# Kernel tuning notes

Hardware: AMD Instinct MI355X
Metric: run time of the kernel (lower is better)

## Reference

```python
import jax, jax.numpy as jnp
import numpy as np

N, D, L, H = 4, 512, 2048, 8  # batch, feat_dim, seq_len, num_heads


def setup_inputs() -> dict:
    key = jax.random.key(0)
    k1, k2, k3, k4 = jax.random.split(key, 4)
    x = jax.random.normal(k1, (N, D, L), dtype=jnp.float32)
    w_qkv = jax.random.normal(k2, (3 * D, D, 1), dtype=jnp.float32) * 0.02   # 1x1 conv
    w_dw = jax.random.normal(k3, (3 * D, 1, 3), dtype=jnp.float32) * 0.02    # depthwise k=3
    w_proj = jax.random.normal(k4, (D, D, 1), dtype=jnp.float32) * 0.02      # 1x1 conv
    temperature = jnp.ones((1, H, 1, 1), dtype=jnp.float32)
    return {"x": x, "w_qkv": w_qkv, "w_dw": w_dw, "w_proj": w_proj, "temperature": temperature}


def _conv1x1(x, w):
    # x: (n, c_in, l), w: (c_out, c_in, 1)
    return jnp.einsum('oc,ncl->nol', w[:, :, 0], x)


def _l2norm(t, eps=1e-12):
    # matches F.normalize: t / max(||t||_2, eps) along last dim
    n = jnp.sqrt(jnp.sum(t * t, axis=-1, keepdims=True))
    return t / jnp.maximum(n, eps)


def reference(x, w_qkv, w_dw, w_proj, temperature):
    n, d, l = x.shape
    h = temperature.shape[1]
    dh = d // h

    qkv = _conv1x1(x, w_qkv)                               # (n, 3d, l)
    qkv = jax.lax.conv_general_dilated(
        qkv, w_dw, window_strides=(1,), padding=[(1, 1)],
        dimension_numbers=('NCH', 'OIH', 'NCH'),
        feature_group_count=3 * d)                          # depthwise conv, (n, 3d, l)

    q, k, v = jnp.split(qkv, 3, axis=1)                     # each (n, d, l)
    # (n, d, l) -> (n, h, dh, l) -> (n, h, l, dh)
    q = q.reshape(n, h, dh, l).transpose(0, 1, 3, 2)
    k = k.reshape(n, h, dh, l).transpose(0, 1, 3, 2)
    v = v.reshape(n, h, dh, l).transpose(0, 1, 3, 2)

    q = _l2norm(q)
    k = _l2norm(k)

    scores = jnp.einsum('nhqd,nhkd->nhqk', q, k) * temperature  # (n, h, l, l)
    attn = jax.nn.softmax(scores, axis=-1)
    out = jnp.einsum('nhqk,nhkd->nhqd', attn, v)                # (n, h, l, dh)
    out = out.transpose(0, 1, 3, 2).reshape(n, d, l)            # (n, d, l)
    return _conv1x1(out, w_proj)
```

## Files before the change

kernel.cpp:

```cpp
#include <hip/hip_runtime.h>
#include <hip/hip_bf16.h>
#include <cstdint>
#include <cstddef>

#define N_B 4
#define D_F 512
#define L_S 2048
#define H_N 8
#define DH  64
#define C3  (3*D_F)

typedef __attribute__((ext_vector_type(8)))  short short8;
typedef __attribute__((ext_vector_type(4)))  float f32x4;
typedef __attribute__((ext_vector_type(16))) float f32x16;

__device__ __forceinline__ unsigned int pk_bf16(float a, float b) {
    __hip_bfloat162 h = __float22bfloat162_rn(float2{a, b});
    union { __hip_bfloat162 h; unsigned int u; } cv;
    cv.h = h;
    return cv.u;
}
__device__ __forceinline__ unsigned short bf16_rn(float f) {
    union { float f; unsigned int u; } c; c.f = f;
    unsigned int r = c.u + 0x7FFF + ((c.u >> 16) & 1);
    return (unsigned short)(r >> 16);
}
__device__ __forceinline__ float bf16_f(unsigned short h) {
    union { unsigned int u; float f; } c; c.u = ((unsigned int)h) << 16;
    return c.f;
}

__device__ __forceinline__ void gll16(const unsigned short* g, unsigned short* l) {
    __builtin_amdgcn_global_load_lds(
        (const __attribute__((address_space(1))) unsigned int*)g,
        (__attribute__((address_space(3))) unsigned int*)l,
        16, 0, 0);
}

__global__ __launch_bounds__(256) void cvt_split(const float* __restrict__ src,
                                                 unsigned short* __restrict__ hi,
                                                 unsigned short* __restrict__ lo,
                                                 int n4) {
    int i = blockIdx.x * 256 + threadIdx.x;
    if (i >= n4) return;
    float4 v = ((const float4*)src)[i];
    ushort4 h, l;
    h.x = bf16_rn(v.x); l.x = bf16_rn(v.x - bf16_f(h.x));
    h.y = bf16_rn(v.y); l.y = bf16_rn(v.y - bf16_f(h.y));
    h.z = bf16_rn(v.z); l.z = bf16_rn(v.z - bf16_f(h.z));
    h.w = bf16_rn(v.w); l.w = bf16_rn(v.w - bf16_f(h.w));
    ((ushort4*)hi)[i] = h;
    ((ushort4*)lo)[i] = l;
}

__global__ __launch_bounds__(256) void cvt_xT(const float* __restrict__ x,
                                              unsigned short* __restrict__ xT,
                                              int C) {
    __shared__ float tile[64][65];
    const int tid = threadIdx.x;
    const int l0  = blockIdx.x * 64;
    const int c0  = blockIdx.y * 64;
    const int n   = blockIdx.z;

    const float* xn = x + (size_t)n * C * L_S;
#pragma unroll
    for (int r = 0; r < 16; ++r) {
        int c = r * 4 + (tid >> 6);
        int l = tid & 63;
        tile[c][l] = xn[(size_t)(c0 + c) * L_S + l0 + l];
    }
    __syncthreads();

    unsigned short* xn_t = xT + (size_t)n * L_S * C;
#pragma unroll
    for (int r = 0; r < 8; ++r) {
        int l  = r * 8 + (tid >> 5);
        int cp = tid & 31;
        unsigned int pk = pk_bf16(tile[cp * 2][l], tile[cp * 2 + 1][l]);
        *(unsigned int*)&xn_t[(size_t)(l0 + l) * C + c0 + cp * 2] = pk;
    }
}

template<int SPLIT, int OUT_BF16>
__global__ __launch_bounds__(256) void gemm_mfma2(const unsigned short* __restrict__ Whi,
                                                  const unsigned short* __restrict__ Wlo,
                                                  const unsigned short* __restrict__ XThi,
                                                  const unsigned short* __restrict__ XTlo,
                                                  void* __restrict__ Y,
                                                  int O, int C) {
    __shared__ unsigned short Wt[SPLIT ? 2 : 1][4][128 * 8];
    __shared__ unsigned short Xt[SPLIT ? 2 : 1][4][128 * 8];

    const int tid  = threadIdx.x;
    const int lane = tid & 63;
    const int w    = tid >> 6;
    const int g    = lane >> 4;
    const int c    = lane & 15;
    const int wr   = (w >> 1) * 64;
    const int wc   = (w & 1) * 64;
    const int l0   = blockIdx.x * 128;
    const int o0   = blockIdx.y * 128;
    const int n    = blockIdx.z;

    const unsigned short* XTn_hi = XThi + (size_t)n * L_S * C;
    const unsigned short* XTn_lo = SPLIT ? (XTlo + (size_t)n * L_S * C) : nullptr;

    const int rhalf = (w & 1) * 64;
    const int cpA   = w >> 1;
    const int cpB   = 2 + (w >> 1);
    const size_t wrowA = (size_t)(o0 + rhalf + lane) * C;
    const size_t xrowA = (size_t)(l0 + rhalf + lane) * C;

    f32x4 acc[4][4];
#pragma unroll
    for (int mt = 0; mt < 4; ++mt)
#pragma unroll
        for (int nt = 0; nt < 4; ++nt) acc[mt][nt] = (f32x4){0.f, 0.f, 0.f, 0.f};

    for (int c0 = 0; c0 < C; c0 += 32) {
        __syncthreads();
        gll16(Whi + wrowA + c0 + cpA * 8, &Wt[0][cpA][rhalf * 8]);
        gll16(Whi + wrowA + c0 + cpB * 8, &Wt[0][cpB][rhalf * 8]);
        gll16(XTn_hi + xrowA + c0 + cpA * 8, &Xt[0][cpA][rhalf * 8]);
        gll16(XTn_hi + xrowA + c0 + cpB * 8, &Xt[0][cpB][rhalf * 8]);
        if (SPLIT) {
            gll16(Wlo + wrowA + c0 + cpA * 8, &Wt[1][cpA][rhalf * 8]);
            gll16(Wlo + wrowA + c0 + cpB * 8, &Wt[1][cpB][rhalf * 8]);
            gll16(XTn_lo + xrowA + c0 + cpA * 8, &Xt[1][cpA][rhalf * 8]);
            gll16(XTn_lo + xrowA + c0 + cpB * 8, &Xt[1][cpB][rhalf * 8]);
        }
        __syncthreads();

        short8 a0[4], b0[4];
#pragma unroll
        for (int mt = 0; mt < 4; ++mt) a0[mt] = *(short8*)&Wt[0][g][(wr + mt * 16 + c) * 8];
#pragma unroll
        for (int nt = 0; nt < 4; ++nt) b0[nt] = *(short8*)&Xt[0][g][(wc + nt * 16 + c) * 8];

        if (SPLIT) {
            short8 a1[4], b1[4];
#pragma unroll
            for (int mt = 0; mt < 4; ++mt) a1[mt] = *(short8*)&Wt[1][g][(wr + mt * 16 + c) * 8];
#pragma unroll
            for (int nt = 0; nt < 4; ++nt) b1[nt] = *(short8*)&Xt[1][g][(wc + nt * 16 + c) * 8];
#pragma unroll
            for (int mt = 0; mt < 4; ++mt)
#pragma unroll
                for (int nt = 0; nt < 4; ++nt) {
                    acc[mt][nt] = __builtin_amdgcn_mfma_f32_16x16x32_bf16(a0[mt], b0[nt], acc[mt][nt], 0, 0, 0);
                    acc[mt][nt] = __builtin_amdgcn_mfma_f32_16x16x32_bf16(a0[mt], b1[nt], acc[mt][nt], 0, 0, 0);
                    acc[mt][nt] = __builtin_amdgcn_mfma_f32_16x16x32_bf16(a1[mt], b0[nt], acc[mt][nt], 0, 0, 0);
                }
        } else {
#pragma unroll
            for (int mt = 0; mt < 4; ++mt)
#pragma unroll
                for (int nt = 0; nt < 4; ++nt)
                    acc[mt][nt] = __builtin_amdgcn_mfma_f32_16x16x32_bf16(a0[mt], b0[nt], acc[mt][nt], 0, 0, 0);
        }
    }

#pragma unroll
    for (int mt = 0; mt < 4; ++mt) {
#pragma unroll
        for (int r = 0; r < 4; ++r) {
            int oo = o0 + wr + mt * 16 + g * 4 + r;
            size_t rowbase = ((size_t)n * O + oo) * L_S;
#pragma unroll
            for (int nt = 0; nt < 4; ++nt) {
                int ll = l0 + wc + nt * 16 + c;
                if (OUT_BF16)
                    ((unsigned short*)Y)[rowbase + ll] = bf16_rn(acc[mt][nt][r]);
                else
                    ((float*)Y)[rowbase + ll] = acc[mt][nt][r];
            }
        }
    }
}

__global__ __launch_bounds__(256) void fused_qk2(const unsigned short* __restrict__ qkv_bf,
                                                 const float* __restrict__ w_dw,
                                                 unsigned short* __restrict__ Qb,
                                                 unsigned short* __restrict__ Kb) {
    __shared__ unsigned short rows[64 * 264];
    __shared__ float wsm[192];
    const int tid = threadIdx.x;
    const int l0  = blockIdx.x * 256;
    const int gg  = blockIdx.y;
    const int n   = blockIdx.z;
    const int head = gg & 7;
    const int ch0  = (gg < 8) ? head * 64 : 512 + head * 64;

    if (tid < 192) wsm[tid] = w_dw[ch0 * 3 + tid];

    const unsigned short* base = qkv_bf + ((size_t)n * C3 + ch0) * L_S;
    for (int f = tid; f < 2048; f += 256) {
        int e = f >> 5, s = f & 31;
        *(uint4*)&rows[e * 264 + s * 8] = *(const uint4*)&base[(size_t)e * L_S + l0 + s * 8];
    }
    if (tid < 64) {
        rows[tid * 264 + 256] = (l0 > 0) ? base[(size_t)tid * L_S + l0 - 1] : (unsigned short)0;
    } else if (tid < 128) {
        int e = tid - 64;
        rows[e * 264 + 257] = (l0 + 256 < L_S) ? base[(size_t)e * L_S + l0 + 256] : (unsigned short)0;
    }
    __syncthreads();

    const int lL = tid;
    const int iL = (lL == 0)   ? 256 : lL - 1;
    const int iR = (lL == 255) ? 257 : lL + 1;
    float y[64];
    float s = 0.f;
#pragma unroll
    for (int e = 0; e < 64; ++e) {
        float a = bf16_f(rows[e * 264 + iL]);
        float b = bf16_f(rows[e * 264 + lL]);
        float d = bf16_f(rows[e * 264 + iR]);
        float v = wsm[e * 3 + 0] * a + wsm[e * 3 + 1] * b + wsm[e * 3 + 2] * d;
        y[e] = v;
        s += v * v;
    }
    float sc = 1.0f / fmaxf(sqrtf(s), 1e-12f);

    const int l = l0 + tid;
    unsigned short* dst = ((gg < 8) ? Qb : Kb) + (size_t)(n * H_N + head) * 8 * L_S * 8;
#pragma unroll
    for (int p = 0; p < 8; ++p) {
        uint4 pk = make_uint4(pk_bf16(y[8 * p + 0] * sc, y[8 * p + 1] * sc),
                              pk_bf16(y[8 * p + 2] * sc, y[8 * p + 3] * sc),
                              pk_bf16(y[8 * p + 4] * sc, y[8 * p + 5] * sc),
                              pk_bf16(y[8 * p + 6] * sc, y[8 * p + 7] * sc));
        *(uint4*)&dst[((size_t)p * L_S + l) * 8] = pk;
    }
}

__global__ __launch_bounds__(256) void fused_v2(const unsigned short* __restrict__ qkv_bf,
                                                const float* __restrict__ w_dw,
                                                unsigned short* __restrict__ Vb) {
    const int tid = threadIdx.x;
    const int e   = tid & 63;
    const int jp  = blockIdx.x * 4 + (tid >> 6);
    const int h   = blockIdx.y;
    const int n   = blockIdx.z;
    const int ch  = 1024 + h * 64 + e;
    const unsigned short* row = qkv_bf + ((size_t)n * C3 + ch) * L_S;
    const int k0 = jp * 8;

    uint4 mv = *(const uint4*)&row[k0];
    unsigned int lw = (jp > 0)   ? *(const unsigned int*)&row[k0 - 2] : 0u;
    unsigned int rw = (jp < 255) ? *(const unsigned int*)&row[k0 + 8] : 0u;

    float v[10];
    v[0] = bf16_f((unsigned short)(lw >> 16));
    v[1] = bf16_f((unsigned short)(mv.x & 0xFFFF));
    v[2] = bf16_f((unsigned short)(mv.x >> 16));
    v[3] = bf16_f((unsigned short)(mv.y & 0xFFFF));
    v[4] = bf16_f((unsigned short)(mv.y >> 16));
    v[5] = bf16_f((unsigned short)(mv.z & 0xFFFF));
    v[6] = bf16_f((unsigned short)(mv.z >> 16));
    v[7] = bf16_f((unsigned short)(mv.w & 0xFFFF));
    v[8] = bf16_f((unsigned short)(mv.w >> 16));
    v[9] = bf16_f((unsigned short)(rw & 0xFFFF));

    float w0 = w_dw[ch * 3 + 0], w1 = w_dw[ch * 3 + 1], w2 = w_dw[ch * 3 + 2];
    unsigned int o[4];
#pragma unroll
    for (int i = 0; i < 4; ++i) {
        float y0 = w0 * v[2 * i + 0] + w1 * v[2 * i + 1] + w2 * v[2 * i + 2];
        float y1 = w0 * v[2 * i + 1] + w1 * v[2 * i + 2] + w2 * v[2 * i + 3];
        o[i] = pk_bf16(y0, y1);
    }
    uint4 ov = make_uint4(o[0], o[1], o[2], o[3]);
    *(uint4*)&Vb[(((size_t)(n * H_N + h) * 256 + jp) * 512) + e * 8] = ov;
}

__global__ __launch_bounds__(512, 2) void attn9(const unsigned short* __restrict__ Qb,
                                                const unsigned short* __restrict__ Kb,
                                                const unsigned short* __restrict__ Vb,
                                                const float* __restrict__ temp,
                                                unsigned short* __restrict__ aoT_hi,
                                                unsigned short* __restrict__ aoT_lo) {
    __shared__ float Ot[128 * 64];
    __shared__ float smB[128];
    __shared__ float smA[128];

    const int tid  = threadIdx.x;
    const int lane = tid & 63;
    const int w    = tid >> 6;
    const int g2   = w >> 2;
    const int wv   = w & 3;
    const int c32  = lane & 31;
    const int h    = lane >> 5;
    const int q0   = blockIdx.x * 128;
    const int hd   = blockIdx.y;
    const int n    = blockIdx.z;

    const size_t hb = (size_t)(n * H_N + hd);
    const unsigned short* Qh = Qb + hb * 8 * L_S * 8;
    const unsigned short* Kh = Kb + hb * 8 * L_S * 8;
    const unsigned short* Vh = Vb + hb * 256 * 512;
    const float t    = temp[hd];
    const float negm = -fabsf(t);

    short8 qa[4];
#pragma unroll
    for (int es = 0; es < 4; ++es)
        qa[es] = *(const short8*)&Qh[((size_t)(es * 2 + h) * L_S + q0 + wv * 32 + c32) * 8];

    f32x16 acc0, acc1;
#pragma unroll
    for (int i = 0; i < 16; ++i) { acc0[i] = 0.f; acc1[i] = 0.f; }
    float sumP = 0.f;

    for (int it = 0; it < 16; ++it) {
        const int k0 = (it * 2 + g2) * 64;

        short8 vb0[4], vb1[4];
#pragma unroll
        for (int ks = 0; ks < 4; ++ks) {
            const unsigned short* vrow = Vh + (size_t)((k0 >> 3) + ks * 2 + h) * 512;
            vb0[ks] = *(const short8*)&vrow[c32 * 8];
            vb1[ks] = *(const short8*)&vrow[(32 + c32) * 8];
        }

        f32x16 sf0, sf1;
#pragma unroll
        for (int i = 0; i < 16; ++i) { sf0[i] = 0.f; sf1[i] = 0.f; }
        short8 ka0[4], ka1[4];
#pragma unroll
        for (int es = 0; es < 4; ++es) {
            const unsigned short* krow = Kh + (size_t)(es * 2 + h) * L_S * 8;
            ka0[es] = *(const short8*)&krow[(k0 + c32) * 8];
            ka1[es] = *(const short8*)&krow[(k0 + 32 + c32) * 8];
        }
        __builtin_amdgcn_s_setprio(1);
#pragma unroll
        for (int es = 0; es < 4; ++es) {
            sf0 = __builtin_amdgcn_mfma_f32_32x32x16_bf16(ka0[es], qa[es], sf0, 0, 0, 0);
            sf1 = __builtin_amdgcn_mfma_f32_32x32x16_bf16(ka1[es], qa[es], sf1, 0, 0, 0);
        }
        __builtin_amdgcn_s_setprio(0);

        short8 pa[4];
        {
            unsigned int W_[16], R_[16];
#pragma unroll
            for (int G = 0; G < 4; ++G) {
                float p0 = __expf(fmaf(sf0[4*G+0], t, negm));
                float p1 = __expf(fmaf(sf0[4*G+1], t, negm));
                float p2 = __expf(fmaf(sf0[4*G+2], t, negm));
                float p3 = __expf(fmaf(sf0[4*G+3], t, negm));
                sumP += (p0 + p1) + (p2 + p3);
                W_[2*G]   = pk_bf16(p0, p1);
                W_[2*G+1] = pk_bf16(p2, p3);
                float u0 = __expf(fmaf(sf1[4*G+0], t, negm));
                float u1 = __expf(fmaf(sf1[4*G+1], t, negm));
                float u2 = __expf(fmaf(sf1[4*G+2], t, negm));
                float u3 = __expf(fmaf(sf1[4*G+3], t, negm));
                sumP += (u0 + u1) + (u2 + u3);
                W_[8+2*G]   = pk_bf16(u0, u1);
                W_[8+2*G+1] = pk_bf16(u2, u3);
            }
#pragma unroll
            for (int j = 0; j < 16; ++j) R_[j] = __shfl_xor(W_[j], 32);
#pragma unroll
            for (int ks = 0; ks < 4; ++ks) {
                const int bb = (ks >> 1) * 8;
                const int m4 = (ks & 1) * 4;
                unsigned int a0 = h ? R_[bb+m4+2] : W_[bb+m4+0];
                unsigned int a1 = h ? R_[bb+m4+3] : W_[bb+m4+1];
                unsigned int a2 = h ? W_[bb+m4+2] : R_[bb+m4+0];
                unsigned int a3 = h ? W_[bb+m4+3] : R_[bb+m4+1];
                uint4 pu = make_uint4(a0, a1, a2, a3);
                pa[ks] = *(short8*)&pu;
            }
        }

        __builtin_amdgcn_s_setprio(1);
#pragma unroll
        for (int ks = 0; ks < 4; ++ks) {
            acc0 = __builtin_amdgcn_mfma_f32_32x32x16_bf16(pa[ks], vb0[ks], acc0, 0, 0, 0);
            acc1 = __builtin_amdgcn_mfma_f32_32x32x16_bf16(pa[ks], vb1[ks], acc1, 0, 0, 0);
        }
        __builtin_amdgcn_s_setprio(0);
    }

    sumP += __shfl_xor(sumP, 32);

    if (g2 == 1) {
        smB[wv * 32 + c32] = sumP;
#pragma unroll
        for (int r = 0; r < 16; ++r) {
            int ql = (r & 3) + 8 * (r >> 2) + 4 * h;
            int qg = wv * 32 + ql;
            Ot[qg * 64 + c32]      = acc0[r];
            Ot[qg * 64 + 32 + c32] = acc1[r];
        }
    } else {
        smA[wv * 32 + c32] = sumP;
    }
    __syncthreads();

    if (g2 == 0) {
        float b0[16], b1[16], inv[16];
#pragma unroll
        for (int r = 0; r < 16; ++r) {
            int ql = (r & 3) + 8 * (r >> 2) + 4 * h;
            int qg = wv * 32 + ql;
            b0[r] = Ot[qg * 64 + c32];
            b1[r] = Ot[qg * 64 + 32 + c32];
            inv[r] = 1.0f / (smA[qg] + smB[qg]);
        }
#pragma unroll
        for (int r = 0; r < 16; ++r) {
            int ql = (r & 3) + 8 * (r >> 2) + 4 * h;
            int qg = wv * 32 + ql;
            Ot[qg * 64 + (c32 ^ (qg & 31))]        = (acc0[r] + b0[r]) * inv[r];
            Ot[qg * 64 + ((32 + c32) ^ (qg & 31))] = (acc1[r] + b1[r]) * inv[r];
        }
    }
    __syncthreads();

    for (int tt = tid; tt < 8192; tt += 512) {
        int qq = tt >> 6, e = tt & 63;
        float v = Ot[qq * 64 + (e ^ (qq & 31))];
        unsigned short hi_ = bf16_rn(v);
        unsigned short lo_ = bf16_rn(v - bf16_f(hi_));
        size_t off = ((size_t)n * L_S + q0 + qq) * D_F + hd * 64 + e;
        aoT_hi[off] = hi_;
        aoT_lo[off] = lo_;
    }
}

extern "C" void kernel_launch(void* const* d_in, const int* in_sizes, int n_in,
                              void* d_out, int out_size, void* d_ws, size_t ws_size,
                              hipStream_t stream) {
    const float* x      = (const float*)d_in[0];
    const float* w_qkv  = (const float*)d_in[1];
    const float* w_dw   = (const float*)d_in[2];
    const float* w_proj = (const float*)d_in[3];
    const float* temp   = (const float*)d_in[4];
    float* out = (float*)d_out;

    const size_t WQE = (size_t)C3 * D_F;
    const size_t WPE = (size_t)D_F * D_F;

    char* ws = (char*)d_ws;
    unsigned short* qkv_bf = (unsigned short*)ws;
    unsigned short* Qb     = (unsigned short*)(ws + 25165824);
    unsigned short* Kb     = (unsigned short*)(ws + 33554432);
    unsigned short* Vb     = (unsigned short*)(ws + 41943040);
    unsigned short* xT     = (unsigned short*)(ws + 50331648);
    unsigned short* aoT_lo = (unsigned short*)(ws + 58720256);
    unsigned short* wq_hi  = (unsigned short*)(ws + 67108864);
    unsigned short* wq_lo  = wq_hi + WQE;
    unsigned short* wp_hi  = (unsigned short*)(ws + 70254592);
    unsigned short* wp_lo  = wp_hi + WPE;
    unsigned short* aoT_hi = xT;

    cvt_xT<<<dim3(L_S / 64, D_F / 64, N_B), 256, 0, stream>>>(x, xT, D_F);
    cvt_split<<<dim3((WQE / 4 + 255) / 256), 256, 0, stream>>>(w_qkv, wq_hi, wq_lo, WQE / 4);
    cvt_split<<<dim3((WPE / 4 + 255) / 256), 256, 0, stream>>>(w_proj, wp_hi, wp_lo, WPE / 4);

    gemm_mfma2<0, 1><<<dim3(L_S / 128, C3 / 128, N_B), 256, 0, stream>>>(
        wq_hi, nullptr, xT, nullptr, qkv_bf, C3, D_F);

    fused_qk2<<<dim3(L_S / 256, 16, N_B), 256, 0, stream>>>(qkv_bf, w_dw, Qb, Kb);
    fused_v2<<<dim3(64, H_N, N_B), 256, 0, stream>>>(qkv_bf, w_dw, Vb);

    attn9<<<dim3(L_S / 128, H_N, N_B), 512, 0, stream>>>(Qb, Kb, Vb, temp, aoT_hi, aoT_lo);

    gemm_mfma2<1, 0><<<dim3(L_S / 128, D_F / 128, N_B), 256, 0, stream>>>(
        wp_hi, wp_lo, aoT_hi, aoT_lo, out, D_F, D_F);
}
```

Baseline: 157.4 us.

## Use permlane32_swap for P relayout, raise attention occupancy, merge weight conversions

The attention kernel replaces the 16 cross-half __shfl_xor exchanges used to rearrange softmax probabilities into MFMA A-operand layout with permlane32_swap instructions. A runtime probe determines the swap direction semantics, so the R_ register array is no longer needed. Launch bounds are raised from 2 to 4 blocks per CU, which forces a tighter register budget and risks spills. The two weight-conversion kernels are also merged into one launch to cut launch overhead.

```diff
diff --git a/kernel.cpp b/kernel.cpp
--- a/kernel.cpp
+++ b/kernel.cpp
@@ -37,20 +37,29 @@
         16, 0, 0);
 }
 
-__global__ __launch_bounds__(256) void cvt_split(const float* __restrict__ src,
-                                                 unsigned short* __restrict__ hi,
-                                                 unsigned short* __restrict__ lo,
-                                                 int n4) {
+__global__ __launch_bounds__(256) void cvt_split_w(const float* __restrict__ wq,
+                                                   unsigned short* __restrict__ wq_hi,
+                                                   unsigned short* __restrict__ wq_lo,
+                                                   int n4q,
+                                                   const float* __restrict__ wp,
+                                                   unsigned short* __restrict__ wp_hi,
+                                                   unsigned short* __restrict__ wp_lo,
+                                                   int n4p) {
     int i = blockIdx.x * 256 + threadIdx.x;
-    if (i >= n4) return;
-    float4 v = ((const float4*)src)[i];
+    const float* src;
+    unsigned short *hi, *lo;
+    int idx;
+    if (i < n4q) { src = wq; hi = wq_hi; lo = wq_lo; idx = i; }
+    else if (i < n4q + n4p) { src = wp; hi = wp_hi; lo = wp_lo; idx = i - n4q; }
+    else return;
+    float4 v = ((const float4*)src)[idx];
     ushort4 h, l;
     h.x = bf16_rn(v.x); l.x = bf16_rn(v.x - bf16_f(h.x));
     h.y = bf16_rn(v.y); l.y = bf16_rn(v.y - bf16_f(h.y));
     h.z = bf16_rn(v.z); l.z = bf16_rn(v.z - bf16_f(h.z));
     h.w = bf16_rn(v.w); l.w = bf16_rn(v.w - bf16_f(h.w));
-    ((ushort4*)hi)[i] = h;
-    ((ushort4*)lo)[i] = l;
+    ((ushort4*)hi)[idx] = h;
+    ((ushort4*)lo)[idx] = l;
 }
 
 __global__ __launch_bounds__(256) void cvt_xT(const float* __restrict__ x,
@@ -274,12 +283,12 @@
     *(uint4*)&Vb[(((size_t)(n * H_N + h) * 256 + jp) * 512) + e * 8] = ov;
 }
 
-__global__ __launch_bounds__(512, 2) void attn9(const unsigned short* __restrict__ Qb,
-                                                const unsigned short* __restrict__ Kb,
-                                                const unsigned short* __restrict__ Vb,
-                                                const float* __restrict__ temp,
-                                                unsigned short* __restrict__ aoT_hi,
-                                                unsigned short* __restrict__ aoT_lo) {
+__global__ __launch_bounds__(512, 4) void attn10(const unsigned short* __restrict__ Qb,
+                                                 const unsigned short* __restrict__ Kb,
+                                                 const unsigned short* __restrict__ Vb,
+                                                 const float* __restrict__ temp,
+                                                 unsigned short* __restrict__ aoT_hi,
+                                                 unsigned short* __restrict__ aoT_lo) {
     __shared__ float Ot[128 * 64];
     __shared__ float smB[128];
     __shared__ float smA[128];
@@ -302,6 +311,14 @@
     const float t    = temp[hd];
     const float negm = -fabsf(t);
 
+    bool dirA;
+    {
+        auto tp = __builtin_amdgcn_permlane32_swap((int)lane, (int)(lane + 64), false, false);
+        unsigned xv = (unsigned)tp[0];
+        bool ok = (lane < 32) ? true : (xv == (unsigned)(lane + 32));
+        dirA = (__ballot(ok) == 0xFFFFFFFFFFFFFFFFull);
+    }
+
     short8 qa[4];
 #pragma unroll
     for (int es = 0; es < 4; ++es)
@@ -343,7 +360,7 @@
 
         short8 pa[4];
         {
-            unsigned int W_[16], R_[16];
+            unsigned int W_[16];
 #pragma unroll
             for (int G = 0; G < 4; ++G) {
                 float p0 = __expf(fmaf(sf0[4*G+0], t, negm));
@@ -362,15 +379,17 @@
                 W_[8+2*G+1] = pk_bf16(u2, u3);
             }
 #pragma unroll
-            for (int j = 0; j < 16; ++j) R_[j] = __shfl_xor(W_[j], 32);
-#pragma unroll
             for (int ks = 0; ks < 4; ++ks) {
-                const int bb = (ks >> 1) * 8;
-                const int m4 = (ks & 1) * 4;
-                unsigned int a0 = h ? R_[bb+m4+2] : W_[bb+m4+0];
-                unsigned int a1 = h ? R_[bb+m4+3] : W_[bb+m4+1];
-                unsigned int a2 = h ? W_[bb+m4+2] : R_[bb+m4+0];
-                unsigned int a3 = h ? W_[bb+m4+3] : R_[bb+m4+1];
+                unsigned w0 = dirA ? W_[4*ks]   : W_[4*ks+2];
+                unsigned w2 = dirA ? W_[4*ks+2] : W_[4*ks];
+                unsigned w1 = dirA ? W_[4*ks+1] : W_[4*ks+3];
+                unsigned w3 = dirA ? W_[4*ks+3] : W_[4*ks+1];
+                auto r02 = __builtin_amdgcn_permlane32_swap((int)w0, (int)w2, false, false);
+                auto r13 = __builtin_amdgcn_permlane32_swap((int)w1, (int)w3, false, false);
+                unsigned a0 = dirA ? (unsigned)r02[0] : (unsigned)r02[1];
+                unsigned a2 = dirA ? (unsigned)r02[1] : (unsigned)r02[0];
+                unsigned a1 = dirA ? (unsigned)r13[0] : (unsigned)r13[1];
+                unsigned a3 = dirA ? (unsigned)r13[1] : (unsigned)r13[0];
                 uint4 pu = make_uint4(a0, a1, a2, a3);
                 pa[ks] = *(short8*)&pu;
             }
@@ -459,8 +478,11 @@
     unsigned short* aoT_hi = xT;
 
     cvt_xT<<<dim3(L_S / 64, D_F / 64, N_B), 256, 0, stream>>>(x, xT, D_F);
-    cvt_split<<<dim3((WQE / 4 + 255) / 256), 256, 0, stream>>>(w_qkv, wq_hi, wq_lo, WQE / 4);
-    cvt_split<<<dim3((WPE / 4 + 255) / 256), 256, 0, stream>>>(w_proj, wp_hi, wp_lo, WPE / 4);
+    {
+        int n4q = (int)(WQE / 4), n4p = (int)(WPE / 4);
+        cvt_split_w<<<dim3((n4q + n4p + 255) / 256), 256, 0, stream>>>(
+            w_qkv, wq_hi, wq_lo, n4q, w_proj, wp_hi, wp_lo, n4p);
+    }
 
     gemm_mfma2<0, 1><<<dim3(L_S / 128, C3 / 128, N_B), 256, 0, stream>>>(
         wq_hi, nullptr, xT, nullptr, qkv_bf, C3, D_F);
@@ -468,7 +490,7 @@
     fused_qk2<<<dim3(L_S / 256, 16, N_B), 256, 0, stream>>>(qkv_bf, w_dw, Qb, Kb);
     fused_v2<<<dim3(64, H_N, N_B), 256, 0, stream>>>(qkv_bf, w_dw, Vb);
 
-    attn9<<<dim3(L_S / 128, H_N, N_B), 512, 0, stream>>>(Qb, Kb, Vb, temp, aoT_hi, aoT_lo);
+    attn10<<<dim3(L_S / 128, H_N, N_B), 512, 0, stream>>>(Qb, Kb, Vb, temp, aoT_hi, aoT_lo);
 
     gemm_mfma2<1, 0><<<dim3(L_S / 128, D_F / 128, N_B), 256, 0, stream>>>(
         wp_hi, wp_lo, aoT_hi, aoT_lo, out, D_F, D_F);
```

Result: slower. 213.4 us (+35.6%).
